# Optimization experiments

Measured on AMD Instinct MI355X. Metric: run time of the kernel, lower is better.

Reference implementation:

```python
import jax, jax.numpy as jnp
import numpy as np

# Performer/FAVOR+ style linear attention constants (from module __init__)
A_CONST = 0.1
S_CONST = 1.0
B_CONST = (S_CONST * (1.0 - 4.0 * A_CONST)) ** 0.5  # sqrt(0.6)
C_CONST = -(S_CONST + 1.0) / 2.0                    # -1.0

R = 256     # number of random features
D = 64      # head / feature dim
L = 65536   # sequence length
DV = 64     # value dim
SCALE = 0.125  # keep ||q||^2 ~ 1 so exp stays well-conditioned


def setup_inputs() -> dict:
    key = jax.random.key(0)
    kq, kk, kv, kw = jax.random.split(key, 4)
    Q = jax.random.normal(kq, (D, L), dtype=jnp.float32) * SCALE
    K = jax.random.normal(kk, (D, L), dtype=jnp.float32) * SCALE
    V = jax.random.normal(kv, (L, DV), dtype=jnp.float32)
    W = jax.random.normal(kw, (R, D), dtype=jnp.float32)  # random feature projections
    return {"Q": Q, "K": K, "V": V, "W": W}


def _phi(W, X, c):
    # X: [d, L]; W: [r, d] -> features [r, L]
    d = X.shape[0]
    D_norm = (1.0 - 4.0 * A_CONST) ** (d / 4.0)  # pow(pow(1-4A,0.25), d)
    sq = jnp.sum(X * X, axis=0)                  # [L], diag of X^T X
    return D_norm * jnp.exp(A_CONST + B_CONST * (W @ X) + c * sq)


def reference(Q, K, V, W):
    phiK = _phi(W, K, C_CONST * S_CONST)  # f2: [r, Lk]
    kv = phiK @ V                          # [r, dv]
    phiQ = _phi(W, Q, C_CONST)             # f1: [r, Lq]
    return phiQ.T @ kv                     # [Lq, dv]
```

## Files before the change

### kernel.cpp

```cpp
#include <hip/hip_runtime.h>

typedef _Float16 f16;
typedef __attribute__((ext_vector_type(8))) _Float16 f16x8;
typedef __attribute__((ext_vector_type(4))) _Float16 f16x4;
typedef __attribute__((ext_vector_type(4))) float f32x4;

#define BARRIER()                                              \
    do {                                                       \
        asm volatile("s_waitcnt lgkmcnt(0)" ::: "memory");     \
        __builtin_amdgcn_s_barrier();                          \
        __builtin_amdgcn_sched_barrier(0);                     \
    } while (0)

namespace {
constexpr int kL   = 65536;
constexpr int kR   = 256;
constexpr int kD   = 64;
constexpr int kDV  = 64;

constexpr int kABlocks = 512;
constexpr int kBBlocks = 512;
constexpr int kRBlocks = 128;

constexpr float kBc   = 0.7745966692414834f;
constexpr float kBase0 = -1.1417405264f;
constexpr float kOutScale = 9.5367431640625e-7f;
}

__global__ __launch_bounds__(512, 2)
void favor_kv(const float* __restrict__ Kg, const float* __restrict__ Vg,
              const float* __restrict__ Wg, f16* __restrict__ partials)
{
    __shared__ f16 sXt[2][64 * 64];
    __shared__ f16 sVt[2][64 * 64];
    __shared__ f16 sPhi[256 * 64];
    __shared__ float sRed[2][8 * 64];
    __shared__ float sRedT[2][64];

    const int tid  = threadIdx.x;
    const int w    = tid >> 6;
    const int lane = tid & 63;
    const int l15  = lane & 15;
    const int lhi  = lane >> 4;
    const int blk  = blockIdx.x;
    const int lblk = blk * 128;

    const int scol  = lane;
    const int dbase = w * 8;

    float ka[2][8], va[2][8];
#pragma unroll
    for (int c = 0; c < 2; ++c) {
        const int l0 = lblk + c * 64;
#pragma unroll
        for (int j = 0; j < 8; ++j) ka[c][j] = Kg[(dbase + j) * kL + l0 + scol];
#pragma unroll
        for (int j = 0; j < 8; ++j) va[c][j] = Vg[(size_t)(l0 + dbase + j) * kDV + scol];
    }

    f16x8 wfrag[2][2];
#pragma unroll
    for (int ri = 0; ri < 2; ++ri)
#pragma unroll
        for (int ks = 0; ks < 2; ++ks) {
            const float* p = Wg + (32 * w + 16 * ri + l15) * kD + 32 * ks + 8 * lhi;
            f16x8 v;
#pragma unroll
            for (int j = 0; j < 8; ++j) v[j] = (f16)p[j];
            wfrag[ri][ks] = v;
        }

    f32x4 acc[4][2];
#pragma unroll
    for (int a = 0; a < 4; ++a)
#pragma unroll
        for (int d = 0; d < 2; ++d) { f32x4 z0 = {0.f, 0.f, 0.f, 0.f}; acc[a][d] = z0; }

    const int wr = w >> 1;
    const int wc = w & 1;

    auto stage = [&](int c) {
        float s = 0.f;
        f16x8 hk, hv;
#pragma unroll
        for (int j = 0; j < 8; ++j) {
            const float x = ka[c][j];
            s += x * x;
            hk[j] = (f16)x;
            hv[j] = (f16)va[c][j];
        }
        sRed[c][w * 64 + scol] = s;
        *(f16x8*)&sXt[c][scol * 64 + (dbase ^ ((scol & 7) << 3))] = hk;
        *(f16x8*)&sVt[c][scol * 64 + (dbase ^ ((scol & 7) << 3))] = hv;
    };

    auto norms = [&](int c) {
        float sqv = 0.f;
#pragma unroll
        for (int g = 0; g < 8; ++g) sqv += sRed[c][g * 64 + lane];
        sRedT[c][lane] = sqv;
    };

    auto zphi = [&](int c) {
        f32x4 base4[4];
#pragma unroll
        for (int lf = 0; lf < 4; ++lf) {
            const f32x4 sq4 = *(const f32x4*)&sRedT[c][16 * lf + 4 * lhi];
#pragma unroll
            for (int j = 0; j < 4; ++j) base4[lf][j] = kBase0 - sq4[j];
        }
#pragma unroll
        for (int ri = 0; ri < 2; ++ri) {
            f32x4 z[4];
#pragma unroll
            for (int lf = 0; lf < 4; ++lf) { f32x4 z0 = {0.f, 0.f, 0.f, 0.f}; z[lf] = z0; }
            __builtin_amdgcn_s_setprio(1);
#pragma unroll
            for (int ks = 0; ks < 2; ++ks) {
                f16x8 bfr[4];
#pragma unroll
                for (int lf = 0; lf < 4; ++lf) {
                    const int row = 16 * lf + l15;
                    bfr[lf] = *(const f16x8*)&sXt[c][row * 64 + ((32 * ks + 8 * lhi) ^ ((row & 7) << 3))];
                }
#pragma unroll
                for (int lf = 0; lf < 4; ++lf)
                    z[lf] = __builtin_amdgcn_mfma_f32_16x16x32_f16(bfr[lf], wfrag[ri][ks], z[lf], 0, 0, 0);
            }
            __builtin_amdgcn_s_setprio(0);
            const int r = 32 * w + 16 * ri + l15;
#pragma unroll
            for (int lf = 0; lf < 4; ++lf) {
                f16x4 ph;
#pragma unroll
                for (int j = 0; j < 4; ++j)
                    ph[j] = (f16)__expf(fmaf(z[lf][j], kBc, base4[lf][j]));
                const int lbase = 16 * lf + 4 * lhi;
                *(f16x4*)&sPhi[r * 64 + (lbase ^ ((r & 7) << 3))] = ph;
            }
        }
    };

    auto pv = [&](int c) {
        __builtin_amdgcn_s_setprio(1);
#pragma unroll
        for (int ks = 0; ks < 2; ++ks) {
            f16x8 af[4], bf[2];
#pragma unroll
            for (int ai = 0; ai < 4; ++ai) {
                const int r = 64 * wr + 16 * ai + l15;
                af[ai] = *(const f16x8*)&sPhi[r * 64 + ((32 * ks + 8 * lhi) ^ ((r & 7) << 3))];
            }
#pragma unroll
            for (int di = 0; di < 2; ++di) {
                const int dv = 32 * wc + 16 * di + l15;
                bf[di] = *(const f16x8*)&sVt[c][dv * 64 + ((32 * ks + 8 * lhi) ^ ((dv & 7) << 3))];
            }
#pragma unroll
            for (int ai = 0; ai < 4; ++ai)
#pragma unroll
                for (int di = 0; di < 2; ++di)
                    acc[ai][di] = __builtin_amdgcn_mfma_f32_16x16x32_f16(af[ai], bf[di], acc[ai][di], 0, 0, 0);
        }
        __builtin_amdgcn_s_setprio(0);
    };

    stage(0);
    BARRIER();
    norms(0);
    zphi(0);
    stage(1);
    BARRIER();
    norms(1);
    pv(0);
    BARRIER();
    zphi(1);
    BARRIER();
    pv(1);

    f16* po = partials + (size_t)blk * (kR * kDV);
#pragma unroll
    for (int ai = 0; ai < 4; ++ai)
#pragma unroll
        for (int di = 0; di < 2; ++di) {
            const int dv = 32 * wc + 16 * di + l15;
            f16x4 pk;
#pragma unroll
            for (int j = 0; j < 4; ++j) pk[j] = (f16)acc[ai][di][j];
            *(f16x4*)&po[dv * kR + 64 * wr + 16 * ai + 4 * lhi] = pk;
        }
}

__global__ __launch_bounds__(512)
void favor_reduce(const f16* __restrict__ partials, f16* __restrict__ kvT)
{
    __shared__ float sAcc[32][128];
    const int tid  = threadIdx.x;
    const int slot = tid & 15;
    const int g    = tid >> 4;
    const size_t obase = (size_t)blockIdx.x * 128 + slot * 8;

    float a[8] = {0.f, 0.f, 0.f, 0.f, 0.f, 0.f, 0.f, 0.f};
#pragma unroll 4
    for (int i = 0; i < 16; ++i) {
        const int s = g * 16 + i;
        const f16x8 v = *(const f16x8*)&partials[(size_t)s * (kR * kDV) + obase];
#pragma unroll
        for (int j = 0; j < 8; ++j) a[j] += (float)v[j];
    }
#pragma unroll
    for (int j = 0; j < 8; ++j) sAcc[g][slot * 8 + j] = a[j];
    __syncthreads();

    if (tid < 128) {
        float tot = 0.f;
#pragma unroll
        for (int gg = 0; gg < 32; ++gg) tot += sAcc[gg][tid];
        kvT[(size_t)blockIdx.x * 128 + tid] = (f16)tot;
    }
}

__global__ __launch_bounds__(512, 2)
void favor_out(const float* __restrict__ Qg, const float* __restrict__ Wg,
               const f16* __restrict__ kvT, float* __restrict__ outg)
{
    __shared__ f16 sXt[2][64 * 64];
    __shared__ f16 sPhiT[64 * 256];
    __shared__ float sRed[2][8 * 64];

    const int tid  = threadIdx.x;
    const int w    = tid >> 6;
    const int lane = tid & 63;
    const int l15  = lane & 15;
    const int lhi  = lane >> 4;
    const int blk  = blockIdx.x;
    const int lblk = blk * 128;

    const int scol  = lane;
    const int dbase = w * 8;
    const int lfo = w >> 1;
    const int dvh = w & 1;

    float qa[2][8];
#pragma unroll
    for (int c = 0; c < 2; ++c)
#pragma unroll
        for (int j = 0; j < 8; ++j)
            qa[c][j] = Qg[(dbase + j) * kL + lblk + c * 64 + scol];

    f16x8 kvf[2][8];
#pragma unroll
    for (int di = 0; di < 2; ++di) {
        const int dv = 32 * dvh + 16 * di + l15;
#pragma unroll
        for (int ks = 0; ks < 8; ++ks)
            kvf[di][ks] = *(const f16x8*)&kvT[dv * kR + 32 * ks + 8 * lhi];
    }

    f16x8 wfrag[2][2];
#pragma unroll
    for (int ri = 0; ri < 2; ++ri)
#pragma unroll
        for (int ks = 0; ks < 2; ++ks) {
            const float* p = Wg + (32 * w + 16 * ri + l15) * kD + 32 * ks + 8 * lhi;
            f16x8 v;
#pragma unroll
            for (int j = 0; j < 8; ++j) v[j] = (f16)p[j];
            wfrag[ri][ks] = v;
        }

    auto stageQ = [&](int c) {
        float s = 0.f;
        f16x8 hq;
#pragma unroll
        for (int j = 0; j < 8; ++j) {
            const float x = qa[c][j];
            s += x * x;
            hq[j] = (f16)x;
        }
        sRed[c][w * 64 + scol] = s;
        *(f16x8*)&sXt[c][scol * 64 + (dbase ^ ((scol & 7) << 3))] = hq;
    };

    auto zphiQ = [&](int c) {
        float sqv = 0.f;
#pragma unroll
        for (int g = 0; g < 8; ++g) sqv += sRed[c][g * 64 + lane];
        float tbase[4];
#pragma unroll
        for (int lf = 0; lf < 4; ++lf)
            tbase[lf] = kBase0 - __shfl(sqv, lf * 16 + l15, 64);

#pragma unroll
        for (int ri = 0; ri < 2; ++ri) {
            f32x4 z[4];
#pragma unroll
            for (int lf = 0; lf < 4; ++lf) { f32x4 z0 = {0.f, 0.f, 0.f, 0.f}; z[lf] = z0; }
            __builtin_amdgcn_s_setprio(1);
#pragma unroll
            for (int ks = 0; ks < 2; ++ks) {
                f16x8 bfr[4];
#pragma unroll
                for (int lf = 0; lf < 4; ++lf) {
                    const int row = 16 * lf + l15;
                    bfr[lf] = *(const f16x8*)&sXt[c][row * 64 + ((32 * ks + 8 * lhi) ^ ((row & 7) << 3))];
                }
#pragma unroll
                for (int lf = 0; lf < 4; ++lf)
                    z[lf] = __builtin_amdgcn_mfma_f32_16x16x32_f16(wfrag[ri][ks], bfr[lf], z[lf], 0, 0, 0);
            }
            __builtin_amdgcn_s_setprio(0);
            const int r0 = 32 * w + 16 * ri + 4 * lhi;
#pragma unroll
            for (int lf = 0; lf < 4; ++lf) {
                const int lc = 16 * lf + l15;
                f16x4 ph;
#pragma unroll
                for (int j = 0; j < 4; ++j)
                    ph[j] = (f16)__expf(fmaf(z[lf][j], kBc, tbase[lf]));
                *(f16x4*)&sPhiT[lc * 256 + (r0 ^ ((lc & 7) << 3))] = ph;
            }
        }
    };

    auto pvOut = [&](int c) {
        f32x4 o2[2];
        { f32x4 z0 = {0.f, 0.f, 0.f, 0.f}; o2[0] = z0; o2[1] = z0; }
        const int lrow = 16 * lfo + l15;
        __builtin_amdgcn_s_setprio(1);
#pragma unroll
        for (int ks = 0; ks < 8; ++ks) {
            const f16x8 af = *(const f16x8*)&sPhiT[lrow * 256 + ((32 * ks + 8 * lhi) ^ ((lrow & 7) << 3))];
#pragma unroll
            for (int di = 0; di < 2; ++di)
                o2[di] = __builtin_amdgcn_mfma_f32_16x16x32_f16(af, kvf[di][ks], o2[di], 0, 0, 0);
        }
        __builtin_amdgcn_s_setprio(0);
        const int l0 = lblk + c * 64;
#pragma unroll
        for (int di = 0; di < 2; ++di)
#pragma unroll
            for (int j = 0; j < 4; ++j) {
                const int ll = 16 * lfo + 4 * lhi + j;
                const int dv = 32 * dvh + 16 * di + l15;
                outg[(size_t)(l0 + ll) * kDV + dv] = o2[di][j] * kOutScale;
            }
    };

    stageQ(0);
    BARRIER();
    zphiQ(0);
    stageQ(1);
    BARRIER();
    pvOut(0);
    BARRIER();
    zphiQ(1);
    BARRIER();
    pvOut(1);
}

extern "C" void kernel_launch(void* const* d_in, const int* in_sizes, int n_in,
                              void* d_out, int out_size, void* d_ws, size_t ws_size,
                              hipStream_t stream)
{
    const float* Q = (const float*)d_in[0];
    const float* K = (const float*)d_in[1];
    const float* V = (const float*)d_in[2];
    const float* W = (const float*)d_in[3];
    float* out = (float*)d_out;

    f16* partials = (f16*)d_ws;
    f16* kvT = (f16*)((char*)d_ws + (size_t)kABlocks * kR * kDV * sizeof(f16));

    favor_kv<<<kABlocks, 512, 0, stream>>>(K, V, W, partials);
    favor_reduce<<<kRBlocks, 512, 0, stream>>>(partials, kvT);
    favor_out<<<kBBlocks, 512, 0, stream>>>(Q, W, kvT, out);

    (void)in_sizes; (void)n_in; (void)out_size; (void)ws_size;
}
```

Baseline: 42.66 us.

## Restructure output kernel into per-wave 16-row tiles with prepacked W fragments

```diff
diff --git a/kernel.cpp b/kernel.cpp
--- a/kernel.cpp
+++ b/kernel.cpp
@@ -19,7 +19,7 @@
 constexpr int kDV  = 64;
 
 constexpr int kABlocks = 512;
-constexpr int kBBlocks = 512;
+constexpr int kBBlocks = 1024;
 constexpr int kRBlocks = 128;
 
 constexpr float kBc   = 0.7745966692414834f;
@@ -47,6 +47,8 @@
 
     const int scol  = lane;
     const int dbase = w * 8;
+    const int wr = w >> 1;
+    const int wc = w & 1;
 
     float ka[2][8], va[2][8];
 #pragma unroll
@@ -75,9 +77,6 @@
     for (int a = 0; a < 4; ++a)
 #pragma unroll
         for (int d = 0; d < 2; ++d) { f32x4 z0 = {0.f, 0.f, 0.f, 0.f}; acc[a][d] = z0; }
-
-    const int wr = w >> 1;
-    const int wc = w & 1;
 
     auto stage = [&](int c) {
         float s = 0.f;
@@ -192,14 +191,30 @@
 }
 
 __global__ __launch_bounds__(512)
-void favor_reduce(const f16* __restrict__ partials, f16* __restrict__ kvT)
+void favor_reduce(const f16* __restrict__ partials, f16* __restrict__ kvT,
+                  const float* __restrict__ Wg, f16* __restrict__ Wp)
 {
     __shared__ float sAcc[32][128];
     const int tid  = threadIdx.x;
     const int slot = tid & 15;
     const int g    = tid >> 4;
+
+    if (blockIdx.x == 0) {
+#pragma unroll
+        for (int it = 0; it < 4; ++it) {
+            const int idx   = tid + it * 512;
+            const int fragid = idx >> 6;
+            const int ln     = idx & 63;
+            const int rf = fragid >> 1, ks = fragid & 1;
+            const float* src = Wg + (16 * rf + (ln & 15)) * kD + 32 * ks + 8 * (ln >> 4);
+            f16x8 v;
+#pragma unroll
+            for (int j = 0; j < 8; ++j) v[j] = (f16)src[j];
+            *(f16x8*)&Wp[(size_t)idx * 8] = v;
+        }
+    }
+
     const size_t obase = (size_t)blockIdx.x * 128 + slot * 8;
-
     float a[8] = {0.f, 0.f, 0.f, 0.f, 0.f, 0.f, 0.f, 0.f};
 #pragma unroll 4
     for (int i = 0; i < 16; ++i) {
@@ -220,143 +235,97 @@
     }
 }
 
-__global__ __launch_bounds__(512, 2)
-void favor_out(const float* __restrict__ Qg, const float* __restrict__ Wg,
+__global__ __launch_bounds__(256, 4)
+void favor_out(const float* __restrict__ Qg, const f16* __restrict__ Wp,
                const f16* __restrict__ kvT, float* __restrict__ outg)
 {
-    __shared__ f16 sXt[2][64 * 64];
-    __shared__ f16 sPhiT[64 * 256];
-    __shared__ float sRed[2][8 * 64];
+    __shared__ f16 sPhiW[4][16 * 64];
 
     const int tid  = threadIdx.x;
     const int w    = tid >> 6;
     const int lane = tid & 63;
     const int l15  = lane & 15;
     const int lhi  = lane >> 4;
-    const int blk  = blockIdx.x;
-    const int lblk = blk * 128;
-
-    const int scol  = lane;
-    const int dbase = w * 8;
-    const int lfo = w >> 1;
-    const int dvh = w & 1;
-
-    float qa[2][8];
-#pragma unroll
-    for (int c = 0; c < 2; ++c)
+    const int l0w  = blockIdx.x * 64 + w * 16;
+    const int s8   = (l15 & 7) << 3;
+    f16* myPhi = &sPhiW[w][0];
+
+    float qv[2][8];
+#pragma unroll
+    for (int ks = 0; ks < 2; ++ks)
 #pragma unroll
         for (int j = 0; j < 8; ++j)
-            qa[c][j] = Qg[(dbase + j) * kL + lblk + c * 64 + scol];
-
-    f16x8 kvf[2][8];
-#pragma unroll
-    for (int di = 0; di < 2; ++di) {
-        const int dv = 32 * dvh + 16 * di + l15;
-#pragma unroll
-        for (int ks = 0; ks < 8; ++ks)
-            kvf[di][ks] = *(const f16x8*)&kvT[dv * kR + 32 * ks + 8 * lhi];
-    }
-
-    f16x8 wfrag[2][2];
-#pragma unroll
-    for (int ri = 0; ri < 2; ++ri)
-#pragma unroll
-        for (int ks = 0; ks < 2; ++ks) {
-            const float* p = Wg + (32 * w + 16 * ri + l15) * kD + 32 * ks + 8 * lhi;
-            f16x8 v;
-#pragma unroll
-            for (int j = 0; j < 8; ++j) v[j] = (f16)p[j];
-            wfrag[ri][ks] = v;
-        }
-
-    auto stageQ = [&](int c) {
-        float s = 0.f;
-        f16x8 hq;
-#pragma unroll
-        for (int j = 0; j < 8; ++j) {
-            const float x = qa[c][j];
-            s += x * x;
-            hq[j] = (f16)x;
-        }
-        sRed[c][w * 64 + scol] = s;
-        *(f16x8*)&sXt[c][scol * 64 + (dbase ^ ((scol & 7) << 3))] = hq;
-    };
-
-    auto zphiQ = [&](int c) {
-        float sqv = 0.f;
-#pragma unroll
-        for (int g = 0; g < 8; ++g) sqv += sRed[c][g * 64 + lane];
-        float tbase[4];
-#pragma unroll
-        for (int lf = 0; lf < 4; ++lf)
-            tbase[lf] = kBase0 - __shfl(sqv, lf * 16 + l15, 64);
-
-#pragma unroll
-        for (int ri = 0; ri < 2; ++ri) {
-            f32x4 z[4];
-#pragma unroll
-            for (int lf = 0; lf < 4; ++lf) { f32x4 z0 = {0.f, 0.f, 0.f, 0.f}; z[lf] = z0; }
-            __builtin_amdgcn_s_setprio(1);
-#pragma unroll
-            for (int ks = 0; ks < 2; ++ks) {
-                f16x8 bfr[4];
-#pragma unroll
-                for (int lf = 0; lf < 4; ++lf) {
-                    const int row = 16 * lf + l15;
-                    bfr[lf] = *(const f16x8*)&sXt[c][row * 64 + ((32 * ks + 8 * lhi) ^ ((row & 7) << 3))];
-                }
-#pragma unroll
-                for (int lf = 0; lf < 4; ++lf)
-                    z[lf] = __builtin_amdgcn_mfma_f32_16x16x32_f16(wfrag[ri][ks], bfr[lf], z[lf], 0, 0, 0);
-            }
-            __builtin_amdgcn_s_setprio(0);
-            const int r0 = 32 * w + 16 * ri + 4 * lhi;
-#pragma unroll
-            for (int lf = 0; lf < 4; ++lf) {
-                const int lc = 16 * lf + l15;
-                f16x4 ph;
-#pragma unroll
-                for (int j = 0; j < 4; ++j)
-                    ph[j] = (f16)__expf(fmaf(z[lf][j], kBc, tbase[lf]));
-                *(f16x4*)&sPhiT[lc * 256 + (r0 ^ ((lc & 7) << 3))] = ph;
-            }
-        }
-    };
-
-    auto pvOut = [&](int c) {
-        f32x4 o2[2];
-        { f32x4 z0 = {0.f, 0.f, 0.f, 0.f}; o2[0] = z0; o2[1] = z0; }
-        const int lrow = 16 * lfo + l15;
+            qv[ks][j] = Qg[(32 * ks + 8 * lhi + j) * kL + l0w + l15];
+
+    float sq = 0.f;
+#pragma unroll
+    for (int ks = 0; ks < 2; ++ks)
+#pragma unroll
+        for (int j = 0; j < 8; ++j) sq += qv[ks][j] * qv[ks][j];
+    sq += __shfl_xor(sq, 16);
+    sq += __shfl_xor(sq, 32);
+    const float tbase = kBase0 - sq;
+
+    f16x8 qf[2];
+#pragma unroll
+    for (int ks = 0; ks < 2; ++ks)
+#pragma unroll
+        for (int j = 0; j < 8; ++j) qf[ks][j] = (f16)qv[ks][j];
+
+    f32x4 acc[4];
+#pragma unroll
+    for (int di = 0; di < 4; ++di) { f32x4 z0 = {0.f, 0.f, 0.f, 0.f}; acc[di] = z0; }
+
+#pragma unroll 1
+    for (int q4 = 0; q4 < 4; ++q4) {
+        f16x8 wf[4][2];
+#pragma unroll
+        for (int rfq = 0; rfq < 4; ++rfq)
+#pragma unroll
+            for (int ks = 0; ks < 2; ++ks)
+                wf[rfq][ks] = *(const f16x8*)&Wp[(size_t)((((q4 * 4 + rfq) * 2 + ks) * 64) + lane) * 8];
+
+        f16x8 kvf[4][2];
+#pragma unroll
+        for (int di = 0; di < 4; ++di)
+#pragma unroll
+            for (int kk = 0; kk < 2; ++kk)
+                kvf[di][kk] = *(const f16x8*)&kvT[(16 * di + l15) * kR + q4 * 64 + 32 * kk + 8 * lhi];
+
         __builtin_amdgcn_s_setprio(1);
 #pragma unroll
-        for (int ks = 0; ks < 8; ++ks) {
-            const f16x8 af = *(const f16x8*)&sPhiT[lrow * 256 + ((32 * ks + 8 * lhi) ^ ((lrow & 7) << 3))];
-#pragma unroll
-            for (int di = 0; di < 2; ++di)
-                o2[di] = __builtin_amdgcn_mfma_f32_16x16x32_f16(af, kvf[di][ks], o2[di], 0, 0, 0);
+        for (int rfq = 0; rfq < 4; ++rfq) {
+            f32x4 z = {0.f, 0.f, 0.f, 0.f};
+            z = __builtin_amdgcn_mfma_f32_16x16x32_f16(wf[rfq][0], qf[0], z, 0, 0, 0);
+            z = __builtin_amdgcn_mfma_f32_16x16x32_f16(wf[rfq][1], qf[1], z, 0, 0, 0);
+            f16x4 ph;
+#pragma unroll
+            for (int j = 0; j < 4; ++j)
+                ph[j] = (f16)__expf(fmaf(z[j], kBc, tbase));
+            *(f16x4*)&myPhi[l15 * 64 + ((rfq * 16 + 4 * lhi) ^ s8)] = ph;
         }
         __builtin_amdgcn_s_setprio(0);
-        const int l0 = lblk + c * 64;
-#pragma unroll
-        for (int di = 0; di < 2; ++di)
-#pragma unroll
-            for (int j = 0; j < 4; ++j) {
-                const int ll = 16 * lfo + 4 * lhi + j;
-                const int dv = 32 * dvh + 16 * di + l15;
-                outg[(size_t)(l0 + ll) * kDV + dv] = o2[di][j] * kOutScale;
-            }
-    };
-
-    stageQ(0);
-    BARRIER();
-    zphiQ(0);
-    stageQ(1);
-    BARRIER();
-    pvOut(0);
-    BARRIER();
-    zphiQ(1);
-    BARRIER();
-    pvOut(1);
+
+        asm volatile("s_waitcnt lgkmcnt(0)" ::: "memory");
+        __builtin_amdgcn_sched_barrier(0);
+
+        __builtin_amdgcn_s_setprio(1);
+#pragma unroll
+        for (int kk = 0; kk < 2; ++kk) {
+            const f16x8 pf = *(const f16x8*)&myPhi[l15 * 64 + ((32 * kk + 8 * lhi) ^ s8)];
+#pragma unroll
+            for (int di = 0; di < 4; ++di)
+                acc[di] = __builtin_amdgcn_mfma_f32_16x16x32_f16(pf, kvf[di][kk], acc[di], 0, 0, 0);
+        }
+        __builtin_amdgcn_s_setprio(0);
+        __builtin_amdgcn_sched_barrier(0);
+    }
+
+#pragma unroll
+    for (int di = 0; di < 4; ++di)
+#pragma unroll
+        for (int j = 0; j < 4; ++j)
+            outg[(size_t)(l0w + 4 * lhi + j) * kDV + 16 * di + l15] = acc[di][j] * kOutScale;
 }
 
 extern "C" void kernel_launch(void* const* d_in, const int* in_sizes, int n_in,
@@ -371,10 +340,11 @@
 
     f16* partials = (f16*)d_ws;
     f16* kvT = (f16*)((char*)d_ws + (size_t)kABlocks * kR * kDV * sizeof(f16));
+    f16* Wp  = kvT + (size_t)kR * kDV;
 
     favor_kv<<<kABlocks, 512, 0, stream>>>(K, V, W, partials);
-    favor_reduce<<<kRBlocks, 512, 0, stream>>>(partials, kvT);
-    favor_out<<<kBBlocks, 512, 0, stream>>>(Q, W, kvT, out);
+    favor_reduce<<<kRBlocks, 512, 0, stream>>>(partials, kvT, W, Wp);
+    favor_out<<<kBBlocks, 256, 0, stream>>>(Q, Wp, kvT, out);
 
     (void)in_sizes; (void)n_in; (void)out_size; (void)ws_size;
 }
```

Measured after the change: 49.05 us. +15.0%, slower.

## Fuse reduction and output kernels with atomic-flag handoff to overlap Q feature work

Applied to the files above, without the earlier changes.

```diff
diff --git a/kernel.cpp b/kernel.cpp
--- a/kernel.cpp
+++ b/kernel.cpp
@@ -18,9 +18,9 @@
 constexpr int kD   = 64;
 constexpr int kDV  = 64;
 
-constexpr int kABlocks = 512;
-constexpr int kBBlocks = 512;
-constexpr int kRBlocks = 128;
+constexpr int kABlocks  = 512;
+constexpr int kRedBlocks = 128;
+constexpr int kWrkBlocks = 512;
 
 constexpr float kBc   = 0.7745966692414834f;
 constexpr float kBase0 = -1.1417405264f;
@@ -29,8 +29,12 @@
 
 __global__ __launch_bounds__(512, 2)
 void favor_kv(const float* __restrict__ Kg, const float* __restrict__ Vg,
-              const float* __restrict__ Wg, f16* __restrict__ partials)
+              const float* __restrict__ Wg, f16* __restrict__ partials,
+              unsigned* __restrict__ done)
 {
+    if (blockIdx.x == 0 && threadIdx.x == 0)
+        __hip_atomic_store(done, 0u, __ATOMIC_RELAXED, __HIP_MEMORY_SCOPE_AGENT);
+
     __shared__ f16 sXt[2][64 * 64];
     __shared__ f16 sVt[2][64 * 64];
     __shared__ f16 sPhi[256 * 64];
@@ -47,6 +51,8 @@
 
     const int scol  = lane;
     const int dbase = w * 8;
+    const int wr = w >> 1;
+    const int wc = w & 1;
 
     float ka[2][8], va[2][8];
 #pragma unroll
@@ -75,9 +81,6 @@
     for (int a = 0; a < 4; ++a)
 #pragma unroll
         for (int d = 0; d < 2; ++d) { f32x4 z0 = {0.f, 0.f, 0.f, 0.f}; acc[a][d] = z0; }
-
-    const int wr = w >> 1;
-    const int wc = w & 1;
 
     auto stage = [&](int c) {
         float s = 0.f;
@@ -191,49 +194,61 @@
         }
 }
 
-__global__ __launch_bounds__(512)
-void favor_reduce(const f16* __restrict__ partials, f16* __restrict__ kvT)
+__global__ __launch_bounds__(512, 2)
+void favor_rb(const float* __restrict__ Qg, const float* __restrict__ Wg,
+              const f16* __restrict__ partials, f16* __restrict__ kvT,
+              unsigned* __restrict__ done, float* __restrict__ outg)
 {
-    __shared__ float sAcc[32][128];
+    __shared__ union {
+        struct {
+            f16 sXt[2][64 * 64];
+            f16 sPhiT[64 * 256];
+            float sRed[2][8 * 64];
+        } w;
+        struct {
+            float sAcc[32][128];
+        } r;
+    } sm;
+
     const int tid  = threadIdx.x;
-    const int slot = tid & 15;
-    const int g    = tid >> 4;
-    const size_t obase = (size_t)blockIdx.x * 128 + slot * 8;
-
-    float a[8] = {0.f, 0.f, 0.f, 0.f, 0.f, 0.f, 0.f, 0.f};
+
+    if (blockIdx.x < kRedBlocks) {
+        const int slot = tid & 15;
+        const int g    = tid >> 4;
+        const size_t obase = (size_t)blockIdx.x * 128 + slot * 8;
+
+        float a[8] = {0.f, 0.f, 0.f, 0.f, 0.f, 0.f, 0.f, 0.f};
 #pragma unroll 4
-    for (int i = 0; i < 16; ++i) {
-        const int s = g * 16 + i;
-        const f16x8 v = *(const f16x8*)&partials[(size_t)s * (kR * kDV) + obase];
-#pragma unroll
-        for (int j = 0; j < 8; ++j) a[j] += (float)v[j];
+        for (int i = 0; i < 16; ++i) {
+            const int s = g * 16 + i;
+            const f16x8 v = *(const f16x8*)&partials[(size_t)s * (kR * kDV) + obase];
+#pragma unroll
+            for (int j = 0; j < 8; ++j) a[j] += (float)v[j];
+        }
+#pragma unroll
+        for (int j = 0; j < 8; ++j) sm.r.sAcc[g][slot * 8 + j] = a[j];
+        __syncthreads();
+
+        if (tid < 128) {
+            float tot = 0.f;
+#pragma unroll
+            for (int gg = 0; gg < 32; ++gg) tot += sm.r.sAcc[gg][tid];
+            kvT[(size_t)blockIdx.x * 128 + tid] = (f16)tot;
+        }
+        __syncthreads();
+        if (tid == 0) {
+            __threadfence();
+            __hip_atomic_fetch_add(done, 1u, __ATOMIC_RELEASE,
+                                   __HIP_MEMORY_SCOPE_AGENT);
+        }
+        return;
     }
-#pragma unroll
-    for (int j = 0; j < 8; ++j) sAcc[g][slot * 8 + j] = a[j];
-    __syncthreads();
-
-    if (tid < 128) {
-        float tot = 0.f;
-#pragma unroll
-        for (int gg = 0; gg < 32; ++gg) tot += sAcc[gg][tid];
-        kvT[(size_t)blockIdx.x * 128 + tid] = (f16)tot;
-    }
-}
-
-__global__ __launch_bounds__(512, 2)
-void favor_out(const float* __restrict__ Qg, const float* __restrict__ Wg,
-               const f16* __restrict__ kvT, float* __restrict__ outg)
-{
-    __shared__ f16 sXt[2][64 * 64];
-    __shared__ f16 sPhiT[64 * 256];
-    __shared__ float sRed[2][8 * 64];
-
-    const int tid  = threadIdx.x;
+
     const int w    = tid >> 6;
     const int lane = tid & 63;
     const int l15  = lane & 15;
     const int lhi  = lane >> 4;
-    const int blk  = blockIdx.x;
+    const int blk  = blockIdx.x - kRedBlocks;
     const int lblk = blk * 128;
 
     const int scol  = lane;
@@ -248,15 +263,6 @@
         for (int j = 0; j < 8; ++j)
             qa[c][j] = Qg[(dbase + j) * kL + lblk + c * 64 + scol];
 
-    f16x8 kvf[2][8];
-#pragma unroll
-    for (int di = 0; di < 2; ++di) {
-        const int dv = 32 * dvh + 16 * di + l15;
-#pragma unroll
-        for (int ks = 0; ks < 8; ++ks)
-            kvf[di][ks] = *(const f16x8*)&kvT[dv * kR + 32 * ks + 8 * lhi];
-    }
-
     f16x8 wfrag[2][2];
 #pragma unroll
     for (int ri = 0; ri < 2; ++ri)
@@ -278,14 +284,14 @@
             s += x * x;
             hq[j] = (f16)x;
         }
-        sRed[c][w * 64 + scol] = s;
-        *(f16x8*)&sXt[c][scol * 64 + (dbase ^ ((scol & 7) << 3))] = hq;
+        sm.w.sRed[c][w * 64 + scol] = s;
+        *(f16x8*)&sm.w.sXt[c][scol * 64 + (dbase ^ ((scol & 7) << 3))] = hq;
     };
 
     auto zphiQ = [&](int c) {
         float sqv = 0.f;
 #pragma unroll
-        for (int g = 0; g < 8; ++g) sqv += sRed[c][g * 64 + lane];
+        for (int g = 0; g < 8; ++g) sqv += sm.w.sRed[c][g * 64 + lane];
         float tbase[4];
 #pragma unroll
         for (int lf = 0; lf < 4; ++lf)
@@ -303,7 +309,7 @@
 #pragma unroll
                 for (int lf = 0; lf < 4; ++lf) {
                     const int row = 16 * lf + l15;
-                    bfr[lf] = *(const f16x8*)&sXt[c][row * 64 + ((32 * ks + 8 * lhi) ^ ((row & 7) << 3))];
+                    bfr[lf] = *(const f16x8*)&sm.w.sXt[c][row * 64 + ((32 * ks + 8 * lhi) ^ ((row & 7) << 3))];
                 }
 #pragma unroll
                 for (int lf = 0; lf < 4; ++lf)
@@ -318,10 +324,36 @@
 #pragma unroll
                 for (int j = 0; j < 4; ++j)
                     ph[j] = (f16)__expf(fmaf(z[lf][j], kBc, tbase[lf]));
-                *(f16x4*)&sPhiT[lc * 256 + (r0 ^ ((lc & 7) << 3))] = ph;
-            }
-        }
-    };
+                *(f16x4*)&sm.w.sPhiT[lc * 256 + (r0 ^ ((lc & 7) << 3))] = ph;
+            }
+        }
+    };
+
+    stageQ(0);
+    BARRIER();
+    zphiQ(0);
+    stageQ(1);
+
+    if (tid == 0) {
+        while (__hip_atomic_load(done, __ATOMIC_ACQUIRE,
+                                 __HIP_MEMORY_SCOPE_AGENT) < (unsigned)kRedBlocks)
+            __builtin_amdgcn_s_sleep(8);
+    }
+    __syncthreads();
+    {
+        unsigned v = __hip_atomic_load(done, __ATOMIC_ACQUIRE,
+                                       __HIP_MEMORY_SCOPE_AGENT);
+        asm volatile("" ::"v"(v));
+    }
+
+    f16x8 kvf[2][8];
+#pragma unroll
+    for (int di = 0; di < 2; ++di) {
+        const int dv = 32 * dvh + 16 * di + l15;
+#pragma unroll
+        for (int ks = 0; ks < 8; ++ks)
+            kvf[di][ks] = *(const f16x8*)&kvT[dv * kR + 32 * ks + 8 * lhi];
+    }
 
     auto pvOut = [&](int c) {
         f32x4 o2[2];
@@ -330,7 +362,7 @@
         __builtin_amdgcn_s_setprio(1);
 #pragma unroll
         for (int ks = 0; ks < 8; ++ks) {
-            const f16x8 af = *(const f16x8*)&sPhiT[lrow * 256 + ((32 * ks + 8 * lhi) ^ ((lrow & 7) << 3))];
+            const f16x8 af = *(const f16x8*)&sm.w.sPhiT[lrow * 256 + ((32 * ks + 8 * lhi) ^ ((lrow & 7) << 3))];
 #pragma unroll
             for (int di = 0; di < 2; ++di)
                 o2[di] = __builtin_amdgcn_mfma_f32_16x16x32_f16(af, kvf[di][ks], o2[di], 0, 0, 0);
@@ -347,11 +379,6 @@
             }
     };
 
-    stageQ(0);
-    BARRIER();
-    zphiQ(0);
-    stageQ(1);
-    BARRIER();
     pvOut(0);
     BARRIER();
     zphiQ(1);
@@ -371,10 +398,11 @@
 
     f16* partials = (f16*)d_ws;
     f16* kvT = (f16*)((char*)d_ws + (size_t)kABlocks * kR * kDV * sizeof(f16));
-
-    favor_kv<<<kABlocks, 512, 0, stream>>>(K, V, W, partials);
-    favor_reduce<<<kRBlocks, 512, 0, stream>>>(partials, kvT);
-    favor_out<<<kBBlocks, 512, 0, stream>>>(Q, W, kvT, out);
+    unsigned* done = (unsigned*)((char*)d_ws + (size_t)kABlocks * kR * kDV * sizeof(f16)
+                                 + (size_t)kR * kDV * sizeof(f16));
+
+    favor_kv<<<kABlocks, 512, 0, stream>>>(K, V, W, partials, done);
+    favor_rb<<<kRedBlocks + kWrkBlocks, 512, 0, stream>>>(Q, W, partials, kvT, done, out);
 
     (void)in_sizes; (void)n_in; (void)out_size; (void)ws_size;
 }
```

After: 85.25 us. 99.8% more time.

## Prepack W fragments as f16 in reduce kernel, hoist LDS loads, split MFMA chains

Applied to the files above, without the earlier changes.

```diff
diff --git a/kernel.cpp b/kernel.cpp
--- a/kernel.cpp
+++ b/kernel.cpp
@@ -47,6 +47,8 @@
 
     const int scol  = lane;
     const int dbase = w * 8;
+    const int wr = w >> 1;
+    const int wc = w & 1;
 
     float ka[2][8], va[2][8];
 #pragma unroll
@@ -75,9 +77,6 @@
     for (int a = 0; a < 4; ++a)
 #pragma unroll
         for (int d = 0; d < 2; ++d) { f32x4 z0 = {0.f, 0.f, 0.f, 0.f}; acc[a][d] = z0; }
-
-    const int wr = w >> 1;
-    const int wc = w & 1;
 
     auto stage = [&](int c) {
         float s = 0.f;
@@ -102,13 +101,14 @@
     };
 
     auto zphi = [&](int c) {
-        f32x4 base4[4];
-#pragma unroll
-        for (int lf = 0; lf < 4; ++lf) {
-            const f32x4 sq4 = *(const f32x4*)&sRedT[c][16 * lf + 4 * lhi];
-#pragma unroll
-            for (int j = 0; j < 4; ++j) base4[lf][j] = kBase0 - sq4[j];
-        }
+        f16x8 bfr[2][4];
+#pragma unroll
+        for (int ks = 0; ks < 2; ++ks)
+#pragma unroll
+            for (int lf = 0; lf < 4; ++lf) {
+                const int row = 16 * lf + l15;
+                bfr[ks][lf] = *(const f16x8*)&sXt[c][row * 64 + ((32 * ks + 8 * lhi) ^ ((row & 7) << 3))];
+            }
 #pragma unroll
         for (int ri = 0; ri < 2; ++ri) {
             f32x4 z[4];
@@ -116,25 +116,19 @@
             for (int lf = 0; lf < 4; ++lf) { f32x4 z0 = {0.f, 0.f, 0.f, 0.f}; z[lf] = z0; }
             __builtin_amdgcn_s_setprio(1);
 #pragma unroll
-            for (int ks = 0; ks < 2; ++ks) {
-                f16x8 bfr[4];
-#pragma unroll
-                for (int lf = 0; lf < 4; ++lf) {
-                    const int row = 16 * lf + l15;
-                    bfr[lf] = *(const f16x8*)&sXt[c][row * 64 + ((32 * ks + 8 * lhi) ^ ((row & 7) << 3))];
-                }
+            for (int ks = 0; ks < 2; ++ks)
 #pragma unroll
                 for (int lf = 0; lf < 4; ++lf)
-                    z[lf] = __builtin_amdgcn_mfma_f32_16x16x32_f16(bfr[lf], wfrag[ri][ks], z[lf], 0, 0, 0);
-            }
+                    z[lf] = __builtin_amdgcn_mfma_f32_16x16x32_f16(bfr[ks][lf], wfrag[ri][ks], z[lf], 0, 0, 0);
             __builtin_amdgcn_s_setprio(0);
             const int r = 32 * w + 16 * ri + l15;
 #pragma unroll
             for (int lf = 0; lf < 4; ++lf) {
+                const f32x4 sq4 = *(const f32x4*)&sRedT[c][16 * lf + 4 * lhi];
                 f16x4 ph;
 #pragma unroll
                 for (int j = 0; j < 4; ++j)
-                    ph[j] = (f16)__expf(fmaf(z[lf][j], kBc, base4[lf][j]));
+                    ph[j] = (f16)__expf(fmaf(z[lf][j], kBc, kBase0 - sq4[j]));
                 const int lbase = 16 * lf + 4 * lhi;
                 *(f16x4*)&sPhi[r * 64 + (lbase ^ ((r & 7) << 3))] = ph;
             }
@@ -192,14 +186,30 @@
 }
 
 __global__ __launch_bounds__(512)
-void favor_reduce(const f16* __restrict__ partials, f16* __restrict__ kvT)
+void favor_reduce(const f16* __restrict__ partials, f16* __restrict__ kvT,
+                  const float* __restrict__ Wg, f16* __restrict__ Wp)
 {
     __shared__ float sAcc[32][128];
     const int tid  = threadIdx.x;
     const int slot = tid & 15;
     const int g    = tid >> 4;
+
+    if (blockIdx.x == 0) {
+#pragma unroll
+        for (int it = 0; it < 4; ++it) {
+            const int idx    = tid + it * 512;
+            const int fragid = idx >> 6;
+            const int ln     = idx & 63;
+            const int rf = fragid >> 1, ks = fragid & 1;
+            const float* src = Wg + (16 * rf + (ln & 15)) * kD + 32 * ks + 8 * (ln >> 4);
+            f16x8 v;
+#pragma unroll
+            for (int j = 0; j < 8; ++j) v[j] = (f16)src[j];
+            *(f16x8*)&Wp[(size_t)idx * 8] = v;
+        }
+    }
+
     const size_t obase = (size_t)blockIdx.x * 128 + slot * 8;
-
     float a[8] = {0.f, 0.f, 0.f, 0.f, 0.f, 0.f, 0.f, 0.f};
 #pragma unroll 4
     for (int i = 0; i < 16; ++i) {
@@ -221,7 +231,7 @@
 }
 
 __global__ __launch_bounds__(512, 2)
-void favor_out(const float* __restrict__ Qg, const float* __restrict__ Wg,
+void favor_out(const float* __restrict__ Qg, const f16* __restrict__ Wp,
                const f16* __restrict__ kvT, float* __restrict__ outg)
 {
     __shared__ f16 sXt[2][64 * 64];
@@ -261,13 +271,8 @@
 #pragma unroll
     for (int ri = 0; ri < 2; ++ri)
 #pragma unroll
-        for (int ks = 0; ks < 2; ++ks) {
-            const float* p = Wg + (32 * w + 16 * ri + l15) * kD + 32 * ks + 8 * lhi;
-            f16x8 v;
-#pragma unroll
-            for (int j = 0; j < 8; ++j) v[j] = (f16)p[j];
-            wfrag[ri][ks] = v;
-        }
+        for (int ks = 0; ks < 2; ++ks)
+            wfrag[ri][ks] = *(const f16x8*)&Wp[(size_t)((((2 * w + ri) * 2 + ks) * 64) + lane) * 8];
 
     auto stageQ = [&](int c) {
         float s = 0.f;
@@ -291,6 +296,14 @@
         for (int lf = 0; lf < 4; ++lf)
             tbase[lf] = kBase0 - __shfl(sqv, lf * 16 + l15, 64);
 
+        f16x8 bfr[2][4];
+#pragma unroll
+        for (int ks = 0; ks < 2; ++ks)
+#pragma unroll
+            for (int lf = 0; lf < 4; ++lf) {
+                const int row = 16 * lf + l15;
+                bfr[ks][lf] = *(const f16x8*)&sXt[c][row * 64 + ((32 * ks + 8 * lhi) ^ ((row & 7) << 3))];
+            }
 #pragma unroll
         for (int ri = 0; ri < 2; ++ri) {
             f32x4 z[4];
@@ -298,17 +311,10 @@
             for (int lf = 0; lf < 4; ++lf) { f32x4 z0 = {0.f, 0.f, 0.f, 0.f}; z[lf] = z0; }
             __builtin_amdgcn_s_setprio(1);
 #pragma unroll
-            for (int ks = 0; ks < 2; ++ks) {
-                f16x8 bfr[4];
-#pragma unroll
-                for (int lf = 0; lf < 4; ++lf) {
-                    const int row = 16 * lf + l15;
-                    bfr[lf] = *(const f16x8*)&sXt[c][row * 64 + ((32 * ks + 8 * lhi) ^ ((row & 7) << 3))];
-                }
+            for (int ks = 0; ks < 2; ++ks)
 #pragma unroll
                 for (int lf = 0; lf < 4; ++lf)
-                    z[lf] = __builtin_amdgcn_mfma_f32_16x16x32_f16(wfrag[ri][ks], bfr[lf], z[lf], 0, 0, 0);
-            }
+                    z[lf] = __builtin_amdgcn_mfma_f32_16x16x32_f16(wfrag[ri][ks], bfr[ks][lf], z[lf], 0, 0, 0);
             __builtin_amdgcn_s_setprio(0);
             const int r0 = 32 * w + 16 * ri + 4 * lhi;
 #pragma unroll
@@ -324,27 +330,32 @@
     };
 
     auto pvOut = [&](int c) {
-        f32x4 o2[2];
-        { f32x4 z0 = {0.f, 0.f, 0.f, 0.f}; o2[0] = z0; o2[1] = z0; }
+        f32x4 oA[2], oB[2];
+        { f32x4 z0 = {0.f, 0.f, 0.f, 0.f}; oA[0] = z0; oA[1] = z0; oB[0] = z0; oB[1] = z0; }
         const int lrow = 16 * lfo + l15;
         __builtin_amdgcn_s_setprio(1);
 #pragma unroll
-        for (int ks = 0; ks < 8; ++ks) {
-            const f16x8 af = *(const f16x8*)&sPhiT[lrow * 256 + ((32 * ks + 8 * lhi) ^ ((lrow & 7) << 3))];
-#pragma unroll
-            for (int di = 0; di < 2; ++di)
-                o2[di] = __builtin_amdgcn_mfma_f32_16x16x32_f16(af, kvf[di][ks], o2[di], 0, 0, 0);
+        for (int ks = 0; ks < 4; ++ks) {
+            const f16x8 afA = *(const f16x8*)&sPhiT[lrow * 256 + ((32 * ks + 8 * lhi) ^ ((lrow & 7) << 3))];
+            const f16x8 afB = *(const f16x8*)&sPhiT[lrow * 256 + ((32 * (ks + 4) + 8 * lhi) ^ ((lrow & 7) << 3))];
+#pragma unroll
+            for (int di = 0; di < 2; ++di) {
+                oA[di] = __builtin_amdgcn_mfma_f32_16x16x32_f16(afA, kvf[di][ks], oA[di], 0, 0, 0);
+                oB[di] = __builtin_amdgcn_mfma_f32_16x16x32_f16(afB, kvf[di][ks + 4], oB[di], 0, 0, 0);
+            }
         }
         __builtin_amdgcn_s_setprio(0);
         const int l0 = lblk + c * 64;
 #pragma unroll
-        for (int di = 0; di < 2; ++di)
+        for (int di = 0; di < 2; ++di) {
+            const f32x4 o2 = oA[di] + oB[di];
 #pragma unroll
             for (int j = 0; j < 4; ++j) {
                 const int ll = 16 * lfo + 4 * lhi + j;
                 const int dv = 32 * dvh + 16 * di + l15;
-                outg[(size_t)(l0 + ll) * kDV + dv] = o2[di][j] * kOutScale;
-            }
+                outg[(size_t)(l0 + ll) * kDV + dv] = o2[j] * kOutScale;
+            }
+        }
     };
 
     stageQ(0);
@@ -371,10 +382,11 @@
 
     f16* partials = (f16*)d_ws;
     f16* kvT = (f16*)((char*)d_ws + (size_t)kABlocks * kR * kDV * sizeof(f16));
+    f16* Wp  = kvT + (size_t)kR * kDV;
 
     favor_kv<<<kABlocks, 512, 0, stream>>>(K, V, W, partials);
-    favor_reduce<<<kRBlocks, 512, 0, stream>>>(partials, kvT);
-    favor_out<<<kBBlocks, 512, 0, stream>>>(Q, W, kvT, out);
+    favor_reduce<<<kRBlocks, 512, 0, stream>>>(partials, kvT, W, Wp);
+    favor_out<<<kBBlocks, 512, 0, stream>>>(Q, Wp, kvT, out);
 
     (void)in_sizes; (void)n_in; (void)out_size; (void)ws_size;
 }
```

Result: no change. 42.70 us (+0.1%).
